# Kernel optimization log

Hardware: AMD Instinct MI355X
Metric: run time of the kernel (lower is better)

The kernel has to match this reference:

```python
import jax, jax.numpy as jnp
import numpy as np

B = 8192
N_CLASSES = 1024
MARGIN = 0.1
THRESH = 0.5
SCALE_POS = 2.0
SCALE_NEG = 40.0
EPS = 1e-5


def setup_inputs() -> dict:
    key = jax.random.key(0)
    k1, k2 = jax.random.split(key)
    # cosine-similarity-like values in [-1, 1]
    sim_mat = jax.random.uniform(k1, (B, B), dtype=jnp.float32, minval=-1.0, maxval=1.0)
    labels = jax.random.randint(k2, (B,), 0, N_CLASSES, dtype=jnp.int64)
    return {"sim_mat": sim_mat, "labels": labels}


def reference(sim_mat, labels):
    # [B, B] pair masks
    same = labels[:, None] == labels[None, :]
    pos_mask = same & (sim_mat < 1.0 - EPS)        # positives, excluding self-sim ~ 1
    neg_mask = ~same

    # per-row hardest positive (min) / hardest negative (max); inf sentinels when empty
    min_pos = jnp.min(jnp.where(pos_mask, sim_mat, jnp.inf), axis=1)   # [B]
    max_neg = jnp.max(jnp.where(neg_mask, sim_mat, -jnp.inf), axis=1)  # [B]

    # pair mining: keep informative pairs only
    sel_neg = neg_mask & (sim_mat + MARGIN > min_pos[:, None])
    sel_pos = pos_mask & (sim_mat - MARGIN < max_neg[:, None])

    valid = jnp.any(sel_neg, axis=1) & jnp.any(sel_pos, axis=1)  # rows contributing to loss

    # masked soft-plus style logsumexp losses (sim bounded in [-1,1], exp is safe)
    pos_sum = jnp.sum(jnp.where(sel_pos, jnp.exp(-SCALE_POS * (sim_mat - THRESH)), 0.0), axis=1)
    neg_sum = jnp.sum(jnp.where(sel_neg, jnp.exp(SCALE_NEG * (sim_mat - THRESH)), 0.0), axis=1)
    pos_loss = jnp.log1p(pos_sum) / SCALE_POS
    neg_loss = jnp.log1p(neg_sum) / SCALE_NEG

    loss = jnp.sum(jnp.where(valid, pos_loss + neg_loss, 0.0)) / sim_mat.shape[0]
    return loss
```

## Files before the change

kernel.cpp:

```cpp
#include <hip/hip_runtime.h>
#include <math.h>

namespace {
constexpr int   kB        = 8192;
constexpr int   kBlock    = 256;
constexpr int   kVec      = 4;
constexpr int   kChunks   = kB / (kBlock * kVec);
constexpr int   kRows     = 8;
constexpr int   kGrid     = kB / kRows;
constexpr float kMargin   = 0.1f;
constexpr float kThresh   = 0.5f;
constexpr float kScalePos = 2.0f;
constexpr float kScaleNeg = 40.0f;
constexpr float kEps      = 1e-5f;
}

__global__ __launch_bounds__(kBlock, 4) void ms_loss_kernel(
    const float* __restrict__ sim,
    const int*   __restrict__ labels,
    float*       __restrict__ out)
{
  const int tid      = threadIdx.x;
  const int wave     = tid >> 6;
  const int lane     = tid & 63;
  const int base_row = blockIdx.x * kRows;

  int4 lab[kChunks];
  #pragma unroll
  for (int k = 0; k < kChunks; ++k)
    lab[k] = *reinterpret_cast<const int4*>(labels + k * (kBlock * kVec) + tid * kVec);

  unsigned int mask[kRows];
  #pragma unroll
  for (int r = 0; r < kRows; ++r) {
    const int ml = labels[base_row + r];
    unsigned int m = 0;
    #pragma unroll
    for (int k = 0; k < kChunks; ++k) {
      m |= (unsigned)(lab[k].x == ml) << (k * 4 + 0);
      m |= (unsigned)(lab[k].y == ml) << (k * 4 + 1);
      m |= (unsigned)(lab[k].z == ml) << (k * 4 + 2);
      m |= (unsigned)(lab[k].w == ml) << (k * 4 + 3);
    }
    mask[r] = m;
  }

  float4 buf[2][kChunks];
  {
    const float* __restrict__ s0 = sim + (size_t)base_row * kB;
    #pragma unroll
    for (int k = 0; k < kChunks; ++k)
      buf[0][k] = *reinterpret_cast<const float4*>(s0 + k * (kBlock * kVec) + tid * kVec);
  }

  __shared__ float s_min[kBlock / 64];
  __shared__ float s_max[kBlock / 64];
  __shared__ float s_pos[kBlock / 64];
  __shared__ float s_neg[kBlock / 64];

  float block_loss = 0.0f;

  #pragma unroll
  for (int r = 0; r < kRows; ++r) {
    if (r + 1 < kRows) {
      const float* __restrict__ sn = sim + (size_t)(base_row + r + 1) * kB;
      #pragma unroll
      for (int k = 0; k < kChunks; ++k)
        buf[(r + 1) & 1][k] =
            *reinterpret_cast<const float4*>(sn + k * (kBlock * kVec) + tid * kVec);
    }

    const unsigned int m = mask[r];

    float min_pos =  INFINITY;
    float max_neg = -INFINITY;
    #pragma unroll
    for (int k = 0; k < kChunks; ++k) {
      const float4 v = buf[r & 1][k];
      const float xs[4] = {v.x, v.y, v.z, v.w};
      #pragma unroll
      for (int c = 0; c < 4; ++c) {
        const bool  same = (m >> (k * 4 + c)) & 1u;
        const float x = xs[c];
        min_pos = fminf(min_pos, (same && x < 1.0f - kEps) ? x : INFINITY);
        max_neg = fmaxf(max_neg, same ? -INFINITY : x);
      }
    }
    #pragma unroll
    for (int off = 32; off > 0; off >>= 1) {
      min_pos = fminf(min_pos, __shfl_xor(min_pos, off, 64));
      max_neg = fmaxf(max_neg, __shfl_xor(max_neg, off, 64));
    }
    if (lane == 0) { s_min[wave] = min_pos; s_max[wave] = max_neg; }
    __syncthreads();
    min_pos = fminf(fminf(s_min[0], s_min[1]), fminf(s_min[2], s_min[3]));
    max_neg = fmaxf(fmaxf(s_max[0], s_max[1]), fmaxf(s_max[2], s_max[3]));

    float pos_sum = 0.0f, neg_sum = 0.0f;
    #pragma unroll
    for (int k = 0; k < kChunks; ++k) {
      const float4 v = buf[r & 1][k];
      const float xs[4] = {v.x, v.y, v.z, v.w};
      #pragma unroll
      for (int c = 0; c < 4; ++c) {
        const bool  same = (m >> (k * 4 + c)) & 1u;
        const float x = xs[c];
        const float a = same ? -kScalePos : kScaleNeg;
        const float e = __expf(a * (x - kThresh));
        const bool selp = same && (x < 1.0f - kEps) && (x - kMargin < max_neg);
        const bool seln = (!same) && (x + kMargin > min_pos);
        pos_sum += selp ? e : 0.0f;
        neg_sum += seln ? e : 0.0f;
      }
    }
    #pragma unroll
    for (int off = 32; off > 0; off >>= 1) {
      pos_sum += __shfl_xor(pos_sum, off, 64);
      neg_sum += __shfl_xor(neg_sum, off, 64);
    }
    if (lane == 0) { s_pos[wave] = pos_sum; s_neg[wave] = neg_sum; }
    __syncthreads();
    if (tid == 0) {
      pos_sum = (s_pos[0] + s_pos[1]) + (s_pos[2] + s_pos[3]);
      neg_sum = (s_neg[0] + s_neg[1]) + (s_neg[2] + s_neg[3]);
      if (pos_sum > 0.0f && neg_sum > 0.0f) {
        block_loss += log1pf(pos_sum) * (1.0f / kScalePos)
                    + log1pf(neg_sum) * (1.0f / kScaleNeg);
      }
    }
  }

  if (tid == 0 && block_loss != 0.0f) {
    atomicAdd(out, block_loss * (1.0f / (float)kB));
  }
}

extern "C" void kernel_launch(void* const* d_in, const int* in_sizes, int n_in,
                              void* d_out, int out_size, void* d_ws, size_t ws_size,
                              hipStream_t stream) {
  const float* sim    = (const float*)d_in[0];
  const int*   labels = (const int*)d_in[1];
  float*       out    = (float*)d_out;

  hipMemsetAsync(d_out, 0, sizeof(float) * (size_t)out_size, stream);
  ms_loss_kernel<<<dim3(kGrid), dim3(kBlock), 0, stream>>>(sim, labels, out);
}
```

Baseline: 371.2 us.

## Process one row per block instead of eight with manual double buffering

Each block now handles a single row of the similarity matrix, so the grid grows to 8192 blocks and the register double buffer plus per-block label mask arrays go away. Occupancy is raised through launch bounds of 8 blocks per CU. The kernel relies on more resident waves rather than explicit prefetch to hide memory latency. In exchange, labels are reloaded by every block and there are more atomics into the output.

```diff
diff --git a/kernel.cpp b/kernel.cpp
--- a/kernel.cpp
+++ b/kernel.cpp
@@ -6,8 +6,6 @@
 constexpr int   kBlock    = 256;
 constexpr int   kVec      = 4;
 constexpr int   kChunks   = kB / (kBlock * kVec);
-constexpr int   kRows     = 8;
-constexpr int   kGrid     = kB / kRows;
 constexpr float kMargin   = 0.1f;
 constexpr float kThresh   = 0.5f;
 constexpr float kScalePos = 2.0f;
@@ -15,42 +13,36 @@
 constexpr float kEps      = 1e-5f;
 }
 
-__global__ __launch_bounds__(kBlock, 4) void ms_loss_kernel(
+__global__ __launch_bounds__(kBlock, 8) void ms_loss_kernel(
     const float* __restrict__ sim,
     const int*   __restrict__ labels,
     float*       __restrict__ out)
 {
-  const int tid      = threadIdx.x;
-  const int wave     = tid >> 6;
-  const int lane     = tid & 63;
-  const int base_row = blockIdx.x * kRows;
+  const int tid  = threadIdx.x;
+  const int wave = tid >> 6;
+  const int lane = tid & 63;
+  const int row  = blockIdx.x;
 
-  int4 lab[kChunks];
+  const float* __restrict__ srow = sim + (size_t)row * kB;
+  float4 v[kChunks];
   #pragma unroll
   for (int k = 0; k < kChunks; ++k)
-    lab[k] = *reinterpret_cast<const int4*>(labels + k * (kBlock * kVec) + tid * kVec);
+    v[k] = *reinterpret_cast<const float4*>(srow + k * (kBlock * kVec) + tid * kVec);
 
-  unsigned int mask[kRows];
+  const int ml = labels[row];
+  unsigned int m = 0u;
   #pragma unroll
-  for (int r = 0; r < kRows; ++r) {
-    const int ml = labels[base_row + r];
-    unsigned int m = 0;
-    #pragma unroll
-    for (int k = 0; k < kChunks; ++k) {
-      m |= (unsigned)(lab[k].x == ml) << (k * 4 + 0);
-      m |= (unsigned)(lab[k].y == ml) << (k * 4 + 1);
-      m |= (unsigned)(lab[k].z == ml) << (k * 4 + 2);
-      m |= (unsigned)(lab[k].w == ml) << (k * 4 + 3);
-    }
-    mask[r] = m;
-  }
-
-  float4 buf[2][kChunks];
-  {
-    const float* __restrict__ s0 = sim + (size_t)base_row * kB;
-    #pragma unroll
-    for (int k = 0; k < kChunks; ++k)
-      buf[0][k] = *reinterpret_cast<const float4*>(s0 + k * (kBlock * kVec) + tid * kVec);
+  for (int k = 0; k < kChunks; k += 2) {
+    const int4 la = *reinterpret_cast<const int4*>(labels + (k + 0) * (kBlock * kVec) + tid * kVec);
+    const int4 lb = *reinterpret_cast<const int4*>(labels + (k + 1) * (kBlock * kVec) + tid * kVec);
+    m |= (unsigned)(la.x == ml) << ((k + 0) * 4 + 0);
+    m |= (unsigned)(la.y == ml) << ((k + 0) * 4 + 1);
+    m |= (unsigned)(la.z == ml) << ((k + 0) * 4 + 2);
+    m |= (unsigned)(la.w == ml) << ((k + 0) * 4 + 3);
+    m |= (unsigned)(lb.x == ml) << ((k + 1) * 4 + 0);
+    m |= (unsigned)(lb.y == ml) << ((k + 1) * 4 + 1);
+    m |= (unsigned)(lb.z == ml) << ((k + 1) * 4 + 2);
+    m |= (unsigned)(lb.w == ml) << ((k + 1) * 4 + 3);
   }
 
   __shared__ float s_min[kBlock / 64];
@@ -58,80 +50,62 @@
   __shared__ float s_pos[kBlock / 64];
   __shared__ float s_neg[kBlock / 64];
 
-  float block_loss = 0.0f;
-
+  float min_pos =  INFINITY;
+  float max_neg = -INFINITY;
   #pragma unroll
-  for (int r = 0; r < kRows; ++r) {
-    if (r + 1 < kRows) {
-      const float* __restrict__ sn = sim + (size_t)(base_row + r + 1) * kB;
-      #pragma unroll
-      for (int k = 0; k < kChunks; ++k)
-        buf[(r + 1) & 1][k] =
-            *reinterpret_cast<const float4*>(sn + k * (kBlock * kVec) + tid * kVec);
-    }
-
-    const unsigned int m = mask[r];
-
-    float min_pos =  INFINITY;
-    float max_neg = -INFINITY;
+  for (int k = 0; k < kChunks; ++k) {
+    const float4 f = v[k];
+    const float xs[4] = {f.x, f.y, f.z, f.w};
     #pragma unroll
-    for (int k = 0; k < kChunks; ++k) {
-      const float4 v = buf[r & 1][k];
-      const float xs[4] = {v.x, v.y, v.z, v.w};
-      #pragma unroll
-      for (int c = 0; c < 4; ++c) {
-        const bool  same = (m >> (k * 4 + c)) & 1u;
-        const float x = xs[c];
-        min_pos = fminf(min_pos, (same && x < 1.0f - kEps) ? x : INFINITY);
-        max_neg = fmaxf(max_neg, same ? -INFINITY : x);
-      }
-    }
-    #pragma unroll
-    for (int off = 32; off > 0; off >>= 1) {
-      min_pos = fminf(min_pos, __shfl_xor(min_pos, off, 64));
-      max_neg = fmaxf(max_neg, __shfl_xor(max_neg, off, 64));
-    }
-    if (lane == 0) { s_min[wave] = min_pos; s_max[wave] = max_neg; }
-    __syncthreads();
-    min_pos = fminf(fminf(s_min[0], s_min[1]), fminf(s_min[2], s_min[3]));
-    max_neg = fmaxf(fmaxf(s_max[0], s_max[1]), fmaxf(s_max[2], s_max[3]));
-
-    float pos_sum = 0.0f, neg_sum = 0.0f;
-    #pragma unroll
-    for (int k = 0; k < kChunks; ++k) {
-      const float4 v = buf[r & 1][k];
-      const float xs[4] = {v.x, v.y, v.z, v.w};
-      #pragma unroll
-      for (int c = 0; c < 4; ++c) {
-        const bool  same = (m >> (k * 4 + c)) & 1u;
-        const float x = xs[c];
-        const float a = same ? -kScalePos : kScaleNeg;
-        const float e = __expf(a * (x - kThresh));
-        const bool selp = same && (x < 1.0f - kEps) && (x - kMargin < max_neg);
-        const bool seln = (!same) && (x + kMargin > min_pos);
-        pos_sum += selp ? e : 0.0f;
-        neg_sum += seln ? e : 0.0f;
-      }
-    }
-    #pragma unroll
-    for (int off = 32; off > 0; off >>= 1) {
-      pos_sum += __shfl_xor(pos_sum, off, 64);
-      neg_sum += __shfl_xor(neg_sum, off, 64);
-    }
-    if (lane == 0) { s_pos[wave] = pos_sum; s_neg[wave] = neg_sum; }
-    __syncthreads();
-    if (tid == 0) {
-      pos_sum = (s_pos[0] + s_pos[1]) + (s_pos[2] + s_pos[3]);
-      neg_sum = (s_neg[0] + s_neg[1]) + (s_neg[2] + s_neg[3]);
-      if (pos_sum > 0.0f && neg_sum > 0.0f) {
-        block_loss += log1pf(pos_sum) * (1.0f / kScalePos)
-                    + log1pf(neg_sum) * (1.0f / kScaleNeg);
-      }
+    for (int c = 0; c < 4; ++c) {
+      const bool  same = (m >> (k * 4 + c)) & 1u;
+      const float x = xs[c];
+      min_pos = fminf(min_pos, (same && x < 1.0f - kEps) ? x : INFINITY);
+      max_neg = fmaxf(max_neg, same ? -INFINITY : x);
     }
   }
+  #pragma unroll
+  for (int off = 32; off > 0; off >>= 1) {
+    min_pos = fminf(min_pos, __shfl_xor(min_pos, off, 64));
+    max_neg = fmaxf(max_neg, __shfl_xor(max_neg, off, 64));
+  }
+  if (lane == 0) { s_min[wave] = min_pos; s_max[wave] = max_neg; }
+  __syncthreads();
+  min_pos = fminf(fminf(s_min[0], s_min[1]), fminf(s_min[2], s_min[3]));
+  max_neg = fmaxf(fmaxf(s_max[0], s_max[1]), fmaxf(s_max[2], s_max[3]));
 
-  if (tid == 0 && block_loss != 0.0f) {
-    atomicAdd(out, block_loss * (1.0f / (float)kB));
+  float pos_sum = 0.0f, neg_sum = 0.0f;
+  #pragma unroll
+  for (int k = 0; k < kChunks; ++k) {
+    const float4 f = v[k];
+    const float xs[4] = {f.x, f.y, f.z, f.w};
+    #pragma unroll
+    for (int c = 0; c < 4; ++c) {
+      const bool  same = (m >> (k * 4 + c)) & 1u;
+      const float x = xs[c];
+      const float a = same ? -kScalePos : kScaleNeg;
+      const float e = __expf(a * (x - kThresh));
+      const bool selp = same && (x < 1.0f - kEps) && (x - kMargin < max_neg);
+      const bool seln = (!same) && (x + kMargin > min_pos);
+      pos_sum += selp ? e : 0.0f;
+      neg_sum += seln ? e : 0.0f;
+    }
+  }
+  #pragma unroll
+  for (int off = 32; off > 0; off >>= 1) {
+    pos_sum += __shfl_xor(pos_sum, off, 64);
+    neg_sum += __shfl_xor(neg_sum, off, 64);
+  }
+  if (lane == 0) { s_pos[wave] = pos_sum; s_neg[wave] = neg_sum; }
+  __syncthreads();
+  if (tid == 0) {
+    pos_sum = (s_pos[0] + s_pos[1]) + (s_pos[2] + s_pos[3]);
+    neg_sum = (s_neg[0] + s_neg[1]) + (s_neg[2] + s_neg[3]);
+    if (pos_sum > 0.0f && neg_sum > 0.0f) {
+      const float row_loss = log1pf(pos_sum) * (1.0f / kScalePos)
+                           + log1pf(neg_sum) * (1.0f / kScaleNeg);
+      atomicAdd(out, row_loss * (1.0f / (float)kB));
+    }
   }
 }
 
@@ -143,5 +117,5 @@
   float*       out    = (float*)d_out;
 
   hipMemsetAsync(d_out, 0, sizeof(float) * (size_t)out_size, stream);
-  ms_loss_kernel<<<dim3(kGrid), dim3(kBlock), 0, stream>>>(sim, labels, out);
+  ms_loss_kernel<<<dim3(kB), dim3(kBlock), 0, stream>>>(sim, labels, out);
 }
```

After: 389.9 us. 1.05x slower.
